# Kernel optimization log

Hardware: AMD Instinct MI355X
Metric: run time of the kernel (lower is better)

Reference implementation:

```python
import jax, jax.numpy as jnp
import numpy as np

LSTM_SIZE = 64
NUM_OPS = 5
NUM_LAYERS = 7  # 2 warmup anchors + 5 sampled layers (layer_id 2..6)


def _lstm_cell(x, h, c, w_ih, w_hh, b_ih, b_hh):
    # torch LSTMCell gate order: i, f, g, o
    g = x @ w_ih.T + b_ih + h @ w_hh.T + b_hh  # [1, 4*64]
    i, f, gg, o = jnp.split(g, 4, axis=1)
    c2 = jax.nn.sigmoid(f) * c + jax.nn.sigmoid(i) * jnp.tanh(gg)
    h2 = jax.nn.sigmoid(o) * jnp.tanh(c2)
    return h2, c2


def _sampler(embed, w_ih, w_hh, b_ih, b_hh, w_soft, b_soft, b_soft_no_learn,
             w_attn1, w_attn2, v_attn, prev_c, prev_h, use_bias, key):
    keys = jax.random.split(key, 20)  # 5 layers * (2 index + 2 op) samples
    k = 0
    anchors, anchors_w1, arc_seq = [], [], []
    log_prob = jnp.float32(0.0)
    entropy = jnp.float32(0.0)
    inputs = embed[0][None, :]
    # warmup: two anchor slots (anchors are zeros, per original code)
    for _ in range(2):
        prev_h, prev_c = _lstm_cell(inputs, prev_h, prev_c, w_ih, w_hh, b_ih, b_hh)
        anchors.append(jnp.zeros((1, LSTM_SIZE), jnp.float32))
        anchors_w1.append(prev_h @ w_attn1.T)
    for layer_id in range(2, NUM_LAYERS):
        idxs, ops = [], []
        # sample 2 previous-layer indices via tiny attention
        for _ in range(2):
            prev_h, prev_c = _lstm_cell(inputs, prev_h, prev_c, w_ih, w_hh, b_ih, b_hh)
            query = jnp.concatenate(anchors_w1, axis=0)            # [layer_id, 64]
            q = jnp.tanh(query + prev_h @ w_attn2.T)               # broadcast [layer_id, 64]
            logits = (q @ v_attn.T).reshape(layer_id)              # [layer_id]
            logits = logits / 5.0 + 1.1 * jnp.tanh(logits)
            index = jax.random.categorical(keys[k], logits); k += 1
            logp = jax.nn.log_softmax(logits)
            log_prob = log_prob + (-logp[index])
            entropy = entropy + jax.lax.stop_gradient(-jnp.sum(logp * jnp.exp(logp)))
            idxs.append(index)
            A = jnp.concatenate(anchors, axis=0)                   # [layer_id, 64]
            inputs = A[index][None, :]
        # sample 2 ops
        for _ in range(2):
            prev_h, prev_c = _lstm_cell(inputs, prev_h, prev_c, w_ih, w_hh, b_ih, b_hh)
            logits = (prev_h @ w_soft.T + b_soft)                  # [1, 5]
            logits = 1.1 / 2.5 * jnp.tanh(logits / 5.0)
            if use_bias:
                logits = logits + b_soft_no_learn
            logits = logits[0]
            op_id = jax.random.categorical(keys[k], logits); k += 1
            logp = jax.nn.log_softmax(logits)
            log_prob = log_prob + (-logp[op_id])
            entropy = entropy + jax.lax.stop_gradient(-jnp.sum(logp * jnp.exp(logp)))
            ops.append(op_id)
            inputs = embed[op_id + 1][None, :]
        # extra step producing this layer's anchor
        prev_h, prev_c = _lstm_cell(inputs, prev_h, prev_c, w_ih, w_hh, b_ih, b_hh)
        anchors.append(prev_h)
        anchors_w1.append(prev_h @ w_attn1.T)
        inputs = embed[0][None, :]
        # arc layout per layer after in-place fixups: [idx1, op1, idx2, op2]
        arc_seq += [idxs[0], ops[0], idxs[1], ops[1]]
    arc = jnp.stack(arc_seq)
    return arc, entropy, log_prob, prev_c, prev_h


def setup_inputs() -> dict:
    key = jax.random.key(0)
    ks = jax.random.split(key, 9)
    u = lambda k, shape: jax.random.uniform(k, shape, jnp.float32, -0.1, 0.1)
    return {
        "embed": u(ks[0], (6, LSTM_SIZE)),
        "w_ih": u(ks[1], (4 * LSTM_SIZE, LSTM_SIZE)),
        "w_hh": u(ks[2], (4 * LSTM_SIZE, LSTM_SIZE)),
        "b_ih": u(ks[3], (4 * LSTM_SIZE,)),
        "b_hh": u(ks[4], (4 * LSTM_SIZE,)),
        "w_soft": u(ks[5], (NUM_OPS, LSTM_SIZE)),
        "b_soft": jnp.array([[10.0, 10.0, 0.0, 0.0, 0.0]], jnp.float32),
        "b_soft_no_learn": jnp.array([[0.25, 0.25, -0.25, -0.25, -0.25]], jnp.float32),
        "w_attn1": u(ks[6], (LSTM_SIZE, LSTM_SIZE)),
        "w_attn2": u(ks[7], (LSTM_SIZE, LSTM_SIZE)),
        "v_attn": u(ks[8], (1, LSTM_SIZE)),
        "seed": 0,
    }


def reference(embed, w_ih, w_hh, b_ih, b_hh, w_soft, b_soft, b_soft_no_learn,
              w_attn1, w_attn2, v_attn, seed):
    key = jax.random.key(seed)
    k1, k2 = jax.random.split(key)
    zc = jnp.zeros((1, LSTM_SIZE), jnp.float32)
    zh = jnp.zeros((1, LSTM_SIZE), jnp.float32)
    arc1, ent1, lp1, c, h = _sampler(embed, w_ih, w_hh, b_ih, b_hh, w_soft, b_soft,
                                     b_soft_no_learn, w_attn1, w_attn2, v_attn,
                                     zc, zh, True, k1)
    arc2, ent2, lp2, _, _ = _sampler(embed, w_ih, w_hh, b_ih, b_hh, w_soft, b_soft,
                                     b_soft_no_learn, w_attn1, w_attn2, v_attn,
                                     c, h, False, k2)
    return (arc1, arc2, lp1 + lp2, ent1 + ent2)
```

## Files before the change

### kernel.cpp

```cpp
#include <hip/hip_runtime.h>
#include <cstdint>

#ifndef FASTMATH
#define FASTMATH 1
#endif

#define NT 512

__device__ __forceinline__ uint32_t rotl32_(uint32_t v, int d) {
  return (v << d) | (v >> (32 - d));
}

__device__ __forceinline__ void tf2x32(uint32_t k0, uint32_t k1,
                                       uint32_t x0, uint32_t x1,
                                       uint32_t& o0, uint32_t& o1) {
  const uint32_t k2 = k0 ^ k1 ^ 0x1BD11BDAu;
  x0 += k0; x1 += k1;
#define TF4(a,b,c,d) \
  x0 += x1; x1 = rotl32_(x1,a); x1 ^= x0; \
  x0 += x1; x1 = rotl32_(x1,b); x1 ^= x0; \
  x0 += x1; x1 = rotl32_(x1,c); x1 ^= x0; \
  x0 += x1; x1 = rotl32_(x1,d); x1 ^= x0;
  TF4(13,15,26,6)
  x0 += k1; x1 += k2 + 1u;
  TF4(17,29,16,24)
  x0 += k2; x1 += k0 + 2u;
  TF4(13,15,26,6)
  x0 += k0; x1 += k1 + 3u;
  TF4(17,29,16,24)
  x0 += k1; x1 += k2 + 4u;
  TF4(13,15,26,6)
  x0 += k2; x1 += k0 + 5u;
#undef TF4
  o0 = x0; o1 = x1;
}

#if FASTMATH
__device__ __forceinline__ float tanh_(float x) {
  float e = __expf(2.0f * x);
  return 1.0f - __fdividef(2.0f, e + 1.0f);
}
__device__ __forceinline__ float sig_(float x) {
  return __fdividef(1.0f, 1.0f + __expf(-x));
}
#define log_ __logf
#define exp_ __expf
#else
__device__ __forceinline__ float tanh_(float x) { return tanhf(x); }
__device__ __forceinline__ float sig_(float x) { return 0.5f * tanhf(0.5f * x) + 0.5f; }
#define log_ logf
#define exp_ expf
#endif

template <int CTRL>
__device__ __forceinline__ float dppf(float x) {
  return __int_as_float(__builtin_amdgcn_update_dpp(
      0, __float_as_int(x), CTRL, 0xF, 0xF, true));
}
template <int CTRL>
__device__ __forceinline__ int dppi(int x) {
  return __builtin_amdgcn_update_dpp(0, x, CTRL, 0xF, 0xF, true);
}
constexpr int QP1 = 0xB1;
constexpr int QP2 = 0x4E;
constexpr int HM  = 0x141;

__global__ __launch_bounds__(NT, 1)
void nas_controller(const float* __restrict__ embed,
                    const float* __restrict__ w_ih,
                    const float* __restrict__ w_hh,
                    const float* __restrict__ b_ih,
                    const float* __restrict__ b_hh,
                    const float* __restrict__ w_soft,
                    const float* __restrict__ b_soft,
                    const float* __restrict__ b_soft_nl,
                    const float* __restrict__ w_attn1,
                    const float* __restrict__ w_attn2,
                    const float* __restrict__ v_attn,
                    const int* __restrict__ seedp,
                    float* __restrict__ out) {
  const int tid  = threadIdx.x;
  const int lane = tid & 63;
  const int wid  = tid >> 6;
  const int row  = tid >> 1;
  const int half = tid & 1;

  __shared__ __align__(16) float attn1L[64 * 68];
  __shared__ __align__(16) float attn2L[64 * 68];
  __shared__ __align__(16) float wsoftL[5 * 68 + 8];
  __shared__ __align__(16) float vaL[64];
  __shared__ __align__(16) float preQ[13 * 256];
  __shared__ __align__(16) float aw1sL[8 * 68];
  __shared__ __align__(16) float hw2L[64];
  __shared__ __align__(16) float hB[64];
  __shared__ float gates[2][256];
  __shared__ float gL[320];
  __shared__ float lSave[320];
  __shared__ float lgRaw[8];
  __shared__ float lpT[40], entT[40];
  __shared__ int   biSave[40];
  __shared__ float bsoftL[8], bnlL[8];

  float4 wi[8], wh[8];
  {
    const float4* a = reinterpret_cast<const float4*>(w_ih) + row * 16 + half * 8;
#pragma unroll
    for (int j = 0; j < 8; ++j) wi[j] = a[j];
    const float4* b = reinterpret_cast<const float4*>(w_hh) + row * 16 + half * 8;
#pragma unroll
    for (int j = 0; j < 8; ++j) wh[j] = b[j];
  }
  const float bsum = b_ih[row] + b_hh[row];

  for (int i4 = tid; i4 < 1024; i4 += NT) {
    int r = i4 >> 4, c4 = i4 & 15;
    reinterpret_cast<float4*>(attn1L)[r * 17 + c4] =
        reinterpret_cast<const float4*>(w_attn1)[i4];
    reinterpret_cast<float4*>(attn2L)[r * 17 + c4] =
        reinterpret_cast<const float4*>(w_attn2)[i4];
  }
  for (int i = tid; i < 340; i += NT) {
    int r = i / 68, c = i % 68;
    wsoftL[i] = (c < 64) ? w_soft[r * 64 + c] : 0.f;
  }
  if (tid < 64) { vaL[tid] = v_attn[tid]; hB[tid] = 0.f; }
  if (tid < 8) {
    bsoftL[tid] = (tid < 5) ? b_soft[tid] : 0.f;
    bnlL[tid]   = (tid < 5) ? b_soft_nl[tid] : 0.f;
  }
  preQ[6 * 256 + tid] = 0.f;

  if (tid < 320) {
    int s_ = (tid >= 160) ? 1 : 0;
    int rem = tid - s_ * 160;
    int k = rem >> 3, i = rem & 7;
    uint32_t a, b, ka, kb, o0, o1;
    tf2x32(0u, (uint32_t)seedp[0], 0u, (uint32_t)s_, a, b);
    tf2x32(a, b, 0u, (uint32_t)k, ka, kb);
    tf2x32(ka, kb, 0u, (uint32_t)i, o0, o1);
    uint32_t bits = o0 ^ o1;
    const float TINY = 1.1754943508222875e-38f;
    float uu = __uint_as_float((bits >> 9) | 0x3f800000u) - 1.0f;
    uu = uu * (1.0f - TINY) + TINY;
    uu = fmaxf(TINY, uu);
    gL[tid] = -log_(-log_(uu));
  }

#pragma unroll
  for (int e = 0; e < 6; ++e) {
    const float4* x4 = reinterpret_cast<const float4*>(embed + e * 64) + half * 8;
    float a0 = 0, a1 = 0, a2 = 0, a3 = 0;
#pragma unroll
    for (int j = 0; j < 8; ++j) {
      float4 x = x4[j], w = wi[j];
      a0 = fmaf(w.x, x.x, a0); a1 = fmaf(w.y, x.y, a1);
      a2 = fmaf(w.z, x.z, a2); a3 = fmaf(w.w, x.w, a3);
    }
    float acc = (a0 + a1) + (a2 + a3);
    acc += __shfl_xor(acc, 1);
    if (half == 0) preQ[e * 256 + row] = acc;
  }

  __syncthreads();

  if (half == 0) gates[0][row] = preQ[0 * 256 + row] + bsum;
  __syncthreads();

  float creg = 0.f;
  float hacc = 0.f;
  int gp = 0, sIdx = 0;

  auto nonlinR = [&]() {
    float gi = gates[gp][lane], gf = gates[gp][64 + lane];
    float gg = gates[gp][128 + lane], go = gates[gp][192 + lane];
    float c2 = sig_(gf) * creg + sig_(gi) * tanh_(gg);
    float h2 = sig_(go) * tanh_(c2);
    creg = c2;
    hB[lane] = h2;
  };

  auto hdotAcc = [&]() -> float {
    const float4* h4 = reinterpret_cast<const float4*>(hB) + half * 8;
    float a0 = 0, a1 = 0, a2 = 0, a3 = 0;
#pragma unroll
    for (int j = 0; j < 8; ++j) {
      float4 x = h4[j], w = wh[j];
      a0 = fmaf(w.x, x.x, a0); a1 = fmaf(w.y, x.y, a1);
      a2 = fmaf(w.z, x.z, a2); a3 = fmaf(w.w, x.w, a3);
    }
    float acc = (a0 + a1) + (a2 + a3);
    acc += __shfl_xor(acc, 1);
    return acc;
  };

  auto matvecAll = [&](const float* W, float* dst) {
    const int r8 = tid >> 3, q = tid & 7;
    const float4* w4 = reinterpret_cast<const float4*>(W + r8 * 68 + q * 8);
    float4 wa = w4[0], wb = w4[1];
    const float4* h4 = reinterpret_cast<const float4*>(hB) + q * 2;
    float4 ha = h4[0], hb = h4[1];
    float acc = fmaf(wa.x, ha.x, fmaf(wa.y, ha.y, fmaf(wa.z, ha.z, wa.w * ha.w)));
    acc += fmaf(wb.x, hb.x, fmaf(wb.y, hb.y, fmaf(wb.z, hb.z, wb.w * hb.w)));
    acc += __shfl_xor(acc, 1);
    acc += __shfl_xor(acc, 2);
    acc += __shfl_xor(acc, 4);
    if (q == 0) dst[r8] = acc;
  };

  auto anchorPre = [&](int slot) {
    const float4* h4 = reinterpret_cast<const float4*>(hB) + half * 8;
    float a0 = 0, a1 = 0, a2 = 0, a3 = 0;
#pragma unroll
    for (int j = 0; j < 8; ++j) {
      float4 x = h4[j], w = wi[j];
      a0 = fmaf(w.x, x.x, a0); a1 = fmaf(w.y, x.y, a1);
      a2 = fmaf(w.z, x.z, a2); a3 = fmaf(w.w, x.w, a3);
    }
    float acc = (a0 + a1) + (a2 + a3);
    acc += __shfl_xor(acc, 1);
    if (half == 0) preQ[slot * 256 + row] = acc;
  };

  auto doSelR = [&](int n, int k, int mode, float raw, float* op) -> int {
    float l;
    if (lane < n) {
      if (mode == 0) l = raw / 5.0f + 1.1f * tanh_(raw);
      else {
        l = (float)(1.1 / 2.5) * tanh_(raw / 5.0f);
        if (mode == 1) l += bnlL[lane];
      }
    } else l = -INFINITY;
    if (wid == 0 && lane < 8) lSave[(sIdx * 20 + k) * 8 + lane] = l;
    float g = (lane < n) ? gL[sIdx * 160 + k * 8 + lane] : 0.f;
    float v = (lane < n) ? (l + g) : -INFINITY;
    int bi = lane & 7;
#define ARGSTEP(C) { float ov = dppf<C>(v); int oi = dppi<C>(bi); \
    bool tk = (ov > v) || (ov == v && oi < bi); if (tk) { v = ov; bi = oi; } }
    ARGSTEP(QP1) ARGSTEP(QP2) ARGSTEP(HM)
#undef ARGSTEP
    if (wid == 0 && lane == 0) {
      biSave[sIdx * 20 + k] = bi;
      op[0] = (float)bi;
    }
    return __builtin_amdgcn_readfirstlane(bi);
  };

  for (int s = 0; s < 2; ++s) {
    sIdx = s;
    for (int w = 0; w < 2; ++w) {
      nonlinR();
      matvecAll(attn1L, aw1sL + w * 68);
      hacc = hdotAcc();
      if (half == 0) gates[gp ^ 1][row] = hacc + preQ[0 * 256 + row] + bsum;
      __syncthreads(); gp ^= 1;
    }
    int keyk = 0;
    for (int L = 2; L <= 6; ++L) {
      for (int t = 0; t < 2; ++t) {
        nonlinR();
        matvecAll(attn2L, hw2L);
        hacc = hdotAcc();
        __syncthreads();
        if (wid == 0) {
          const int g8 = lane >> 3, j = lane & 7;
          float sacc = 0.f;
          if (g8 < L) {
            const float4* aw = reinterpret_cast<const float4*>(aw1sL + g8 * 68 + j * 8);
            const float4* hq = reinterpret_cast<const float4*>(hw2L + j * 8);
            const float4* vq = reinterpret_cast<const float4*>(vaL + j * 8);
            float4 A0 = aw[0], A1 = aw[1], H0 = hq[0], H1 = hq[1], V0 = vq[0], V1 = vq[1];
            sacc = fmaf(tanh_(A0.x + H0.x), V0.x, sacc);
            sacc = fmaf(tanh_(A0.y + H0.y), V0.y, sacc);
            sacc = fmaf(tanh_(A0.z + H0.z), V0.z, sacc);
            sacc = fmaf(tanh_(A0.w + H0.w), V0.w, sacc);
            sacc = fmaf(tanh_(A1.x + H1.x), V1.x, sacc);
            sacc = fmaf(tanh_(A1.y + H1.y), V1.y, sacc);
            sacc = fmaf(tanh_(A1.z + H1.z), V1.z, sacc);
            sacc = fmaf(tanh_(A1.w + H1.w), V1.w, sacc);
          }
          sacc += dppf<QP1>(sacc); sacc += dppf<QP2>(sacc); sacc += dppf<HM>(sacc);
          if (lane < 8) lgRaw[lane] = __shfl(sacc, lane << 3);
        }
        __syncthreads();
        int sel = doSelR(L, keyk, 0, lgRaw[lane & 7],
                         out + s * 20 + (L - 2) * 4 + t * 2);
        keyk++;
        if (half == 0) gates[gp ^ 1][row] = hacc + preQ[(6 + sel) * 256 + row] + bsum;
        __syncthreads(); gp ^= 1;
      }
      for (int t = 0; t < 2; ++t) {
        nonlinR();
        hacc = hdotAcc();
        const int g8 = lane >> 3, j = lane & 7;
        float sacc = 0.f;
        if (g8 < 5) {
          const float4* wq = reinterpret_cast<const float4*>(wsoftL + g8 * 68 + j * 8);
          float4 wa = wq[0], wb = wq[1];
          const float4* h4 = reinterpret_cast<const float4*>(hB) + j * 2;
          float4 ha = h4[0], hb = h4[1];
          sacc = fmaf(wa.x, ha.x, fmaf(wa.y, ha.y, fmaf(wa.z, ha.z, wa.w * ha.w)));
          sacc += fmaf(wb.x, hb.x, fmaf(wb.y, hb.y, fmaf(wb.z, hb.z, wb.w * hb.w)));
        }
        sacc += dppf<QP1>(sacc); sacc += dppf<QP2>(sacc); sacc += dppf<HM>(sacc);
        float raw = __shfl(sacc, lane << 3) + bsoftL[lane & 7];
        int sel = doSelR(5, keyk, (s == 0) ? 1 : 2, raw,
                         out + s * 20 + (L - 2) * 4 + t * 2 + 1);
        keyk++;
        if (half == 0) gates[gp ^ 1][row] = hacc + preQ[(1 + sel) * 256 + row] + bsum;
        __syncthreads(); gp ^= 1;
      }
      nonlinR();
      matvecAll(attn1L, aw1sL + L * 68);
      anchorPre(6 + L);
      hacc = hdotAcc();
      if (half == 0) gates[gp ^ 1][row] = hacc + preQ[0 * 256 + row] + bsum;
      __syncthreads(); gp ^= 1;
    }
  }

  if (tid < 320) {
    int j = tid >> 3, c = tid & 7;
    float l = lSave[j * 8 + c];
    float mx = l;
    mx = fmaxf(mx, dppf<QP1>(mx)); mx = fmaxf(mx, dppf<QP2>(mx)); mx = fmaxf(mx, dppf<HM>(mx));
    float e = (l == -INFINITY) ? 0.f : exp_(l - mx);
    float ss = e; ss += dppf<QP1>(ss); ss += dppf<QP2>(ss); ss += dppf<HM>(ss);
    float lse = log_(ss);
    float lpi = l - mx - lse;
    float ec = (l == -INFINITY) ? 0.f : lpi * exp_(lpi);
    ec += dppf<QP1>(ec); ec += dppf<QP2>(ec); ec += dppf<HM>(ec);
    if (c == 0) entT[j] = -ec;
    if (c == biSave[j]) lpT[j] = -(l - mx - lse);
  }
  __syncthreads();
  if (tid == 0) {
    float lp = 0.f, ent = 0.f;
    for (int j = 0; j < 40; ++j) { lp += lpT[j]; ent += entT[j]; }
    out[40] = lp; out[41] = ent;
  }
}

extern "C" void kernel_launch(void* const* d_in, const int* in_sizes, int n_in,
                              void* d_out, int out_size, void* d_ws, size_t ws_size,
                              hipStream_t stream) {
  (void)in_sizes; (void)n_in; (void)out_size; (void)d_ws; (void)ws_size;
  nas_controller<<<1, NT, 0, stream>>>(
      (const float*)d_in[0],
      (const float*)d_in[1],
      (const float*)d_in[2],
      (const float*)d_in[3],
      (const float*)d_in[4],
      (const float*)d_in[5],
      (const float*)d_in[6],
      (const float*)d_in[7],
      (const float*)d_in[8],
      (const float*)d_in[9],
      (const float*)d_in[10],
      (const int*)d_in[11],
      (float*)d_out);
}
```

Baseline: 83.61 us.

## Restructure LSTM sampler step so wave 0 runs nonlinearity and selection serially

The gate nonlinearity, attention logits, op logits and argmax selection now run only in wave 0, with input projection and bias added inside the nonlinearity rather than at the hdot write. The step sequence is reordered so selection and the next cell update are chained inside one wave-0 region, which removes the separate lgRaw barrier round-trip. Other waves only do the matvecs and the h-dot. The intent is to cut the number of block-wide barriers and the redundant per-wave nonlinear work on the serial critical path. In exchange, the other waves sit idle while wave 0 works, and srcSlot is tracked only in wave 0.

```diff
diff --git a/kernel.cpp b/kernel.cpp
--- a/kernel.cpp
+++ b/kernel.cpp
@@ -96,7 +96,6 @@
   __shared__ float gates[2][256];
   __shared__ float gL[320];
   __shared__ float lSave[320];
-  __shared__ float lgRaw[8];
   __shared__ float lpT[40], entT[40];
   __shared__ int   biSave[40];
   __shared__ float bsoftL[8], bnlL[8];
@@ -110,7 +109,10 @@
 #pragma unroll
     for (int j = 0; j < 8; ++j) wh[j] = b[j];
   }
-  const float bsum = b_ih[row] + b_hh[row];
+  const float bsi = b_ih[lane] + b_hh[lane];
+  const float bsf = b_ih[64 + lane] + b_hh[64 + lane];
+  const float bsg = b_ih[128 + lane] + b_hh[128 + lane];
+  const float bso = b_ih[192 + lane] + b_hh[192 + lane];
 
   for (int i4 = tid; i4 < 1024; i4 += NT) {
     int r = i4 >> 4, c4 = i4 & 15;
@@ -124,6 +126,7 @@
     wsoftL[i] = (c < 64) ? w_soft[r * 64 + c] : 0.f;
   }
   if (tid < 64) { vaL[tid] = v_attn[tid]; hB[tid] = 0.f; }
+  if (tid < 256) gates[0][tid] = 0.f;
   if (tid < 8) {
     bsoftL[tid] = (tid < 5) ? b_soft[tid] : 0.f;
     bnlL[tid]   = (tid < 5) ? b_soft_nl[tid] : 0.f;
@@ -163,23 +166,23 @@
 
   __syncthreads();
 
-  if (half == 0) gates[0][row] = preQ[0 * 256 + row] + bsum;
-  __syncthreads();
-
   float creg = 0.f;
-  float hacc = 0.f;
   int gp = 0, sIdx = 0;
-
-  auto nonlinR = [&]() {
-    float gi = gates[gp][lane], gf = gates[gp][64 + lane];
-    float gg = gates[gp][128 + lane], go = gates[gp][192 + lane];
+  int srcSlot = 0;
+
+  auto nonlinW0 = [&]() {
+    const float* pq = preQ + srcSlot * 256;
+    float gi = (gates[gp][lane]       + pq[lane])       + bsi;
+    float gf = (gates[gp][64 + lane]  + pq[64 + lane])  + bsf;
+    float gg = (gates[gp][128 + lane] + pq[128 + lane]) + bsg;
+    float go = (gates[gp][192 + lane] + pq[192 + lane]) + bso;
     float c2 = sig_(gf) * creg + sig_(gi) * tanh_(gg);
     float h2 = sig_(go) * tanh_(c2);
     creg = c2;
     hB[lane] = h2;
   };
 
-  auto hdotAcc = [&]() -> float {
+  auto hdotGW = [&]() {
     const float4* h4 = reinterpret_cast<const float4*>(hB) + half * 8;
     float a0 = 0, a1 = 0, a2 = 0, a3 = 0;
 #pragma unroll
@@ -190,7 +193,7 @@
     }
     float acc = (a0 + a1) + (a2 + a3);
     acc += __shfl_xor(acc, 1);
-    return acc;
+    if (half == 0) gates[gp ^ 1][row] = acc;
   };
 
   auto matvecAll = [&](const float* W, float* dst) {
@@ -221,16 +224,8 @@
     if (half == 0) preQ[slot * 256 + row] = acc;
   };
 
-  auto doSelR = [&](int n, int k, int mode, float raw, float* op) -> int {
-    float l;
-    if (lane < n) {
-      if (mode == 0) l = raw / 5.0f + 1.1f * tanh_(raw);
-      else {
-        l = (float)(1.1 / 2.5) * tanh_(raw / 5.0f);
-        if (mode == 1) l += bnlL[lane];
-      }
-    } else l = -INFINITY;
-    if (wid == 0 && lane < 8) lSave[(sIdx * 20 + k) * 8 + lane] = l;
+  auto argmaxSel = [&](int n, int k, float l, float* op) -> int {
+    if (lane < 8) lSave[(sIdx * 20 + k) * 8 + lane] = l;
     float g = (lane < n) ? gL[sIdx * 160 + k * 8 + lane] : 0.f;
     float v = (lane < n) ? (l + g) : -INFINITY;
     int bi = lane & 7;
@@ -238,82 +233,109 @@
     bool tk = (ov > v) || (ov == v && oi < bi); if (tk) { v = ov; bi = oi; } }
     ARGSTEP(QP1) ARGSTEP(QP2) ARGSTEP(HM)
 #undef ARGSTEP
-    if (wid == 0 && lane == 0) {
+    if (lane == 0) {
       biSave[sIdx * 20 + k] = bi;
       op[0] = (float)bi;
     }
     return __builtin_amdgcn_readfirstlane(bi);
   };
 
+  auto idxSel = [&](int n, int k, float* op) -> int {
+    const int g8 = lane >> 3, j = lane & 7;
+    float sacc = 0.f;
+    if (g8 < n) {
+      const float4* aw = reinterpret_cast<const float4*>(aw1sL + g8 * 68 + j * 8);
+      const float4* hq = reinterpret_cast<const float4*>(hw2L + j * 8);
+      const float4* vq = reinterpret_cast<const float4*>(vaL + j * 8);
+      float4 A0 = aw[0], A1 = aw[1], H0 = hq[0], H1 = hq[1], V0 = vq[0], V1 = vq[1];
+      sacc = fmaf(tanh_(A0.x + H0.x), V0.x, sacc);
+      sacc = fmaf(tanh_(A0.y + H0.y), V0.y, sacc);
+      sacc = fmaf(tanh_(A0.z + H0.z), V0.z, sacc);
+      sacc = fmaf(tanh_(A0.w + H0.w), V0.w, sacc);
+      sacc = fmaf(tanh_(A1.x + H1.x), V1.x, sacc);
+      sacc = fmaf(tanh_(A1.y + H1.y), V1.y, sacc);
+      sacc = fmaf(tanh_(A1.z + H1.z), V1.z, sacc);
+      sacc = fmaf(tanh_(A1.w + H1.w), V1.w, sacc);
+    }
+    sacc += dppf<QP1>(sacc); sacc += dppf<QP2>(sacc); sacc += dppf<HM>(sacc);
+    float raw = __shfl(sacc, lane << 3);
+    float l = (lane < n) ? (raw / 5.0f + 1.1f * tanh_(raw)) : -INFINITY;
+    return argmaxSel(n, k, l, op);
+  };
+
+  auto opSel = [&](int k, int mode, float* op) -> int {
+    const int g8 = lane >> 3, j = lane & 7;
+    float sacc = 0.f;
+    if (g8 < 5) {
+      const float4* wq = reinterpret_cast<const float4*>(wsoftL + g8 * 68 + j * 8);
+      float4 wa = wq[0], wb = wq[1];
+      const float4* h4 = reinterpret_cast<const float4*>(hB) + j * 2;
+      float4 ha = h4[0], hb = h4[1];
+      sacc = fmaf(wa.x, ha.x, fmaf(wa.y, ha.y, fmaf(wa.z, ha.z, wa.w * ha.w)));
+      sacc += fmaf(wb.x, hb.x, fmaf(wb.y, hb.y, fmaf(wb.z, hb.z, wb.w * hb.w)));
+    }
+    sacc += dppf<QP1>(sacc); sacc += dppf<QP2>(sacc); sacc += dppf<HM>(sacc);
+    float raw = __shfl(sacc, lane << 3) + bsoftL[lane & 7];
+    float l;
+    if (lane < 5) {
+      l = (float)(1.1 / 2.5) * tanh_(raw / 5.0f);
+      if (mode == 1) l += bnlL[lane];
+    } else l = -INFINITY;
+    return argmaxSel(5, k, l, op);
+  };
+
   for (int s = 0; s < 2; ++s) {
     sIdx = s;
+    const int opMode = (s == 0) ? 1 : 2;
     for (int w = 0; w < 2; ++w) {
-      nonlinR();
+      if (wid == 0) nonlinW0();
+      __syncthreads();
       matvecAll(attn1L, aw1sL + w * 68);
-      hacc = hdotAcc();
-      if (half == 0) gates[gp ^ 1][row] = hacc + preQ[0 * 256 + row] + bsum;
+      hdotGW();
       __syncthreads(); gp ^= 1;
     }
     int keyk = 0;
     for (int L = 2; L <= 6; ++L) {
-      for (int t = 0; t < 2; ++t) {
-        nonlinR();
-        matvecAll(attn2L, hw2L);
-        hacc = hdotAcc();
-        __syncthreads();
-        if (wid == 0) {
-          const int g8 = lane >> 3, j = lane & 7;
-          float sacc = 0.f;
-          if (g8 < L) {
-            const float4* aw = reinterpret_cast<const float4*>(aw1sL + g8 * 68 + j * 8);
-            const float4* hq = reinterpret_cast<const float4*>(hw2L + j * 8);
-            const float4* vq = reinterpret_cast<const float4*>(vaL + j * 8);
-            float4 A0 = aw[0], A1 = aw[1], H0 = hq[0], H1 = hq[1], V0 = vq[0], V1 = vq[1];
-            sacc = fmaf(tanh_(A0.x + H0.x), V0.x, sacc);
-            sacc = fmaf(tanh_(A0.y + H0.y), V0.y, sacc);
-            sacc = fmaf(tanh_(A0.z + H0.z), V0.z, sacc);
-            sacc = fmaf(tanh_(A0.w + H0.w), V0.w, sacc);
-            sacc = fmaf(tanh_(A1.x + H1.x), V1.x, sacc);
-            sacc = fmaf(tanh_(A1.y + H1.y), V1.y, sacc);
-            sacc = fmaf(tanh_(A1.z + H1.z), V1.z, sacc);
-            sacc = fmaf(tanh_(A1.w + H1.w), V1.w, sacc);
-          }
-          sacc += dppf<QP1>(sacc); sacc += dppf<QP2>(sacc); sacc += dppf<HM>(sacc);
-          if (lane < 8) lgRaw[lane] = __shfl(sacc, lane << 3);
-        }
-        __syncthreads();
-        int sel = doSelR(L, keyk, 0, lgRaw[lane & 7],
-                         out + s * 20 + (L - 2) * 4 + t * 2);
-        keyk++;
-        if (half == 0) gates[gp ^ 1][row] = hacc + preQ[(6 + sel) * 256 + row] + bsum;
-        __syncthreads(); gp ^= 1;
+      float* ob = out + s * 20 + (L - 2) * 4;
+      if (wid == 0) nonlinW0();
+      __syncthreads();
+      matvecAll(attn2L, hw2L);
+      hdotGW();
+      __syncthreads(); gp ^= 1;
+      if (wid == 0) {
+        srcSlot = 6 + idxSel(L, keyk, ob + 0);
+        nonlinW0();
       }
-      for (int t = 0; t < 2; ++t) {
-        nonlinR();
-        hacc = hdotAcc();
-        const int g8 = lane >> 3, j = lane & 7;
-        float sacc = 0.f;
-        if (g8 < 5) {
-          const float4* wq = reinterpret_cast<const float4*>(wsoftL + g8 * 68 + j * 8);
-          float4 wa = wq[0], wb = wq[1];
-          const float4* h4 = reinterpret_cast<const float4*>(hB) + j * 2;
-          float4 ha = h4[0], hb = h4[1];
-          sacc = fmaf(wa.x, ha.x, fmaf(wa.y, ha.y, fmaf(wa.z, ha.z, wa.w * ha.w)));
-          sacc += fmaf(wb.x, hb.x, fmaf(wb.y, hb.y, fmaf(wb.z, hb.z, wb.w * hb.w)));
-        }
-        sacc += dppf<QP1>(sacc); sacc += dppf<QP2>(sacc); sacc += dppf<HM>(sacc);
-        float raw = __shfl(sacc, lane << 3) + bsoftL[lane & 7];
-        int sel = doSelR(5, keyk, (s == 0) ? 1 : 2, raw,
-                         out + s * 20 + (L - 2) * 4 + t * 2 + 1);
-        keyk++;
-        if (half == 0) gates[gp ^ 1][row] = hacc + preQ[(1 + sel) * 256 + row] + bsum;
-        __syncthreads(); gp ^= 1;
+      keyk++;
+      __syncthreads();
+      matvecAll(attn2L, hw2L);
+      hdotGW();
+      __syncthreads(); gp ^= 1;
+      if (wid == 0) {
+        srcSlot = 6 + idxSel(L, keyk, ob + 2);
+        nonlinW0();
+        srcSlot = 1 + opSel(keyk + 1, opMode, ob + 1);
       }
-      nonlinR();
+      keyk += 2;
+      __syncthreads();
+      hdotGW();
+      __syncthreads(); gp ^= 1;
+      if (wid == 0) {
+        nonlinW0();
+        srcSlot = 1 + opSel(keyk, opMode, ob + 3);
+      }
+      keyk++;
+      __syncthreads();
+      hdotGW();
+      __syncthreads(); gp ^= 1;
+      if (wid == 0) {
+        nonlinW0();
+        srcSlot = 0;
+      }
+      __syncthreads();
       matvecAll(attn1L, aw1sL + L * 68);
       anchorPre(6 + L);
-      hacc = hdotAcc();
-      if (half == 0) gates[gp ^ 1][row] = hacc + preQ[0 * 256 + row] + bsum;
+      hdotGW();
       __syncthreads(); gp ^= 1;
     }
   }
```

New measurement: 69.70 us. -16.6%, faster.
